# Kernel optimization log

Hardware: AMD Instinct MI355X
Metric: run time of the kernel (lower is better)

## Reference

```python
import jax, jax.numpy as jnp
import numpy as np

N_SAMPLES = 32768   # exp.n_samples = 2**15
N_FRAMES = 128      # exp.n_frames = n_samples // 256
N_EVENTS = 16
MODEL_DIM = 128
N_FREQS = 16        # 2*16 + 1 = 33 pos-encoding features
POS_DIM = 2 * N_FREQS + 1


def pos_encoded(n_frames, n_freqs):
    # linear position in [-pi, pi] plus sin/cos at geometrically spaced freqs
    x = np.linspace(-np.pi, np.pi, n_frames, dtype=np.float32)[:, None]
    feats = [x]
    for i in range(n_freqs):
        feats.append(np.sin((2.0 ** i) * x))
        feats.append(np.cos((2.0 ** i) * x))
    return jnp.asarray(np.concatenate(feats, axis=-1))  # (n_frames, 33)


def hard_softmax_st(x):
    # softmax -> one-hot at argmax (value forced to exactly 1.0), straight-through backward
    sm = jax.nn.softmax(x, axis=-1)
    onehot = jax.nn.one_hot(jnp.argmax(sm, axis=-1), x.shape[-1], dtype=x.dtype)
    return sm + jax.lax.stop_gradient(onehot - sm)


def fft_convolve(env, tf):
    n = env.shape[-1]
    env = jnp.pad(env, ((0, 0), (0, 0), (0, n)))
    tf = jnp.pad(tf, ((0, 0), (0, 0), (0, n)))
    spec = jnp.fft.rfft(env, axis=-1, norm='ortho') * jnp.fft.rfft(tf, axis=-1, norm='ortho')
    return jnp.fft.irfft(spec, axis=-1, norm='ortho')[..., :n]


def setup_inputs() -> dict:
    key = jax.random.key(0)
    k1, k2, k3, k4, k5 = jax.random.split(key, 5)
    B = 32
    time_latent = jax.random.normal(k1, (B * N_EVENTS, MODEL_DIM), jnp.float32)
    stems = jax.random.normal(k2, (B, N_EVENTS, N_SAMPLES), jnp.float32)
    targets = jax.random.normal(k3, (B, N_EVENTS, N_SAMPLES), jnp.float32)
    lim = 1.0 / np.sqrt(MODEL_DIM)
    W = jax.random.uniform(k4, (MODEL_DIM, POS_DIM), jnp.float32, -lim, lim)
    b = jax.random.uniform(k5, (POS_DIM,), jnp.float32, -lim, lim)
    return {"time_latent": time_latent, "stems": stems, "targets": targets, "W": W, "b": b}


def reference(time_latent, stems, targets, W, b):
    # to_pos linear projection: (B*E, 128) -> (B*E, 33)
    p = time_latent @ W + b
    p = p / (jnp.linalg.norm(p, axis=-1, keepdims=True) + 1e-8)
    pos = pos_encoded(N_FRAMES, N_FREQS)
    pos = pos / (jnp.linalg.norm(pos, axis=-1, keepdims=True) + 1e-8)
    sim = p @ pos.T                      # (B*E, n_frames)
    sm = hard_softmax_st(sim)            # one-hot forward, softmax backward
    step = N_SAMPLES // N_FRAMES         # 256
    sparse = jnp.zeros((p.shape[0], N_SAMPLES), p.dtype).at[:, ::step].set(sm)
    sparse = sparse.reshape(-1, N_EVENTS, N_SAMPLES)  # (B, 16, 32768)
    return fft_convolve(sparse, stems)
```

## Files before the change

### kernel.cpp

```cpp
#include <hip/hip_runtime.h>
#include <math.h>

#define N_SAMPLES 32768
#define N_FRAMES  128
#define N_EVENTS  16
#define MODEL_DIM 128
#define N_FREQS   16
#define POS_DIM   33
#define N_ROWS    512


__global__ __launch_bounds__(64) void pos_kernel(float* __restrict__ pos_hat) {
    int f = blockIdx.x;
    int j = threadIdx.x;

    __shared__ float s_feat[POS_DIM];
    __shared__ float s_inv;

    double step = (2.0 * M_PI) / 127.0;
    double xd = -M_PI + (double)f * step;
    if (f == N_FRAMES - 1) xd = M_PI;
    float x = (float)xd;

    if (j < POS_DIM) {
        float v;
        if (j == 0) {
            v = x;
        } else {
            int i = (j - 1) >> 1;
            double arg = ldexp((double)x, i);
            v = (j & 1) ? (float)sin(arg) : (float)cos(arg);
        }
        s_feat[j] = v;
    }
    __syncthreads();

    if (j == 0) {
        double nrm = 0.0;
        for (int k = 0; k < POS_DIM; ++k)
            nrm += (double)s_feat[k] * (double)s_feat[k];
        s_inv = 1.0f / ((float)sqrt(nrm) + 1e-8f);
    }
    __syncthreads();

    if (j < POS_DIM) pos_hat[f * POS_DIM + j] = s_feat[j] * s_inv;
}

__global__ __launch_bounds__(128) void argmax_kernel(
    const float* __restrict__ tl,
    const float* __restrict__ W,
    const float* __restrict__ b,
    const float* __restrict__ pos_hat,
    int* __restrict__ dout)
{
    __shared__ float  s_tl[MODEL_DIM];
    __shared__ float  s_p[POS_DIM];
    __shared__ double sv[N_FRAMES];
    __shared__ int    si[N_FRAMES];

    int row = blockIdx.x;
    int t = threadIdx.x;

    s_tl[t] = tl[(size_t)row * MODEL_DIM + t];
    __syncthreads();

    if (t < POS_DIM) {
        double acc = (double)b[t];
        for (int k = 0; k < MODEL_DIM; ++k)
            acc += (double)s_tl[k] * (double)W[k * POS_DIM + t];
        s_p[t] = (float)acc;
    }
    __syncthreads();

    double s = 0.0;
    for (int j = 0; j < POS_DIM; ++j)
        s += (double)s_p[j] * (double)pos_hat[t * POS_DIM + j];

    sv[t] = s;
    si[t] = t;
    __syncthreads();

    for (int off = 64; off > 0; off >>= 1) {
        if (t < off) {
            double ov = sv[t + off];
            int    oi = si[t + off];
            if (ov > sv[t] || (ov == sv[t] && oi < si[t])) {
                sv[t] = ov;
                si[t] = oi;
            }
        }
        __syncthreads();
    }
    if (t == 0) dout[row] = si[0] * (N_SAMPLES / N_FRAMES);
}

__global__ __launch_bounds__(256) void shift_kernel(
    const float* __restrict__ stems,
    const int*   __restrict__ dvals,
    float*       __restrict__ out)
{
    int row = blockIdx.y;
    int t = (blockIdx.x * 256 + threadIdx.x) * 4;
    int d = dvals[row];

    const float4* src = (const float4*)(stems + (size_t)row * N_SAMPLES);
    float4*       dst = (float4*)(out + (size_t)row * N_SAMPLES);

    float4 v;
    if (t >= d) {
        v = src[(t - d) >> 2];
        const float sc = 1.0f / 256.0f;
        v.x *= sc; v.y *= sc; v.z *= sc; v.w *= sc;
    } else {
        v = make_float4(0.f, 0.f, 0.f, 0.f);
    }
    dst[t >> 2] = v;
}

extern "C" void kernel_launch(void* const* d_in, const int* in_sizes, int n_in,
                              void* d_out, int out_size, void* d_ws, size_t ws_size,
                              hipStream_t stream) {
    const float* tl    = (const float*)d_in[0];
    const float* stems = (const float*)d_in[1];
    const float* W     = (const float*)d_in[3];
    const float* b     = (const float*)d_in[4];
    float* out = (float*)d_out;

    float* pos_hat = (float*)d_ws;
    int*   dvals   = (int*)((char*)d_ws + 32768);

    pos_kernel<<<N_FRAMES, 64, 0, stream>>>(pos_hat);
    argmax_kernel<<<N_ROWS, 128, 0, stream>>>(tl, W, b, pos_hat, dvals);
    shift_kernel<<<dim3(N_SAMPLES / (256 * 4), N_ROWS), 256, 0, stream>>>(stems, dvals, out);
}
```

Baseline: 169.7 us.

## Fuse argmax computation into shift kernel, recomputing per split block

Merges the projection/argmax kernel and the shift-copy kernel into one launch of 1024-thread blocks, with SPLIT blocks per row. Each block recomputes the row's argmax (double-precision matvec and reduction) and then copies its quarter of the shifted, scaled stem. This removes one kernel launch and the global round trip for the shift values. In exchange the argmax work is done four times per row, and the copy cannot start until that serial compute finishes within each block.

```diff
diff --git a/kernel.cpp b/kernel.cpp
--- a/kernel.cpp
+++ b/kernel.cpp
@@ -8,6 +8,7 @@
 #define N_FREQS   16
 #define POS_DIM   33
 #define N_ROWS    512
+#define SPLIT     4
 
 
 __global__ __launch_bounds__(64) void pos_kernel(float* __restrict__ pos_hat) {
@@ -46,22 +47,24 @@
     if (j < POS_DIM) pos_hat[f * POS_DIM + j] = s_feat[j] * s_inv;
 }
 
-__global__ __launch_bounds__(128) void argmax_kernel(
+__global__ __launch_bounds__(1024) void fused_kernel(
     const float* __restrict__ tl,
     const float* __restrict__ W,
     const float* __restrict__ b,
     const float* __restrict__ pos_hat,
-    int* __restrict__ dout)
+    const float* __restrict__ stems,
+    float*       __restrict__ out)
 {
     __shared__ float  s_tl[MODEL_DIM];
     __shared__ float  s_p[POS_DIM];
     __shared__ double sv[N_FRAMES];
     __shared__ int    si[N_FRAMES];
+    __shared__ int    s_d;
 
-    int row = blockIdx.x;
+    int row = blockIdx.y;
     int t = threadIdx.x;
 
-    s_tl[t] = tl[(size_t)row * MODEL_DIM + t];
+    if (t < MODEL_DIM) s_tl[t] = tl[(size_t)row * MODEL_DIM + t];
     __syncthreads();
 
     if (t < POS_DIM) {
@@ -72,12 +75,13 @@
     }
     __syncthreads();
 
-    double s = 0.0;
-    for (int j = 0; j < POS_DIM; ++j)
-        s += (double)s_p[j] * (double)pos_hat[t * POS_DIM + j];
-
-    sv[t] = s;
-    si[t] = t;
+    if (t < N_FRAMES) {
+        double s = 0.0;
+        for (int j = 0; j < POS_DIM; ++j)
+            s += (double)s_p[j] * (double)pos_hat[t * POS_DIM + j];
+        sv[t] = s;
+        si[t] = t;
+    }
     __syncthreads();
 
     for (int off = 64; off > 0; off >>= 1) {
@@ -91,30 +95,27 @@
         }
         __syncthreads();
     }
-    if (t == 0) dout[row] = si[0] * (N_SAMPLES / N_FRAMES);
-}
+    if (t == 0) s_d = si[0] * (N_SAMPLES / N_FRAMES);
+    __syncthreads();
 
-__global__ __launch_bounds__(256) void shift_kernel(
-    const float* __restrict__ stems,
-    const int*   __restrict__ dvals,
-    float*       __restrict__ out)
-{
-    int row = blockIdx.y;
-    int t = (blockIdx.x * 256 + threadIdx.x) * 4;
-    int d = dvals[row];
-
+    int d = s_d;
     const float4* src = (const float4*)(stems + (size_t)row * N_SAMPLES);
     float4*       dst = (float4*)(out + (size_t)row * N_SAMPLES);
+    const float sc = 1.0f / 256.0f;
 
-    float4 v;
-    if (t >= d) {
-        v = src[(t - d) >> 2];
-        const float sc = 1.0f / 256.0f;
-        v.x *= sc; v.y *= sc; v.z *= sc; v.w *= sc;
-    } else {
-        v = make_float4(0.f, 0.f, 0.f, 0.f);
+    int base = blockIdx.x * (N_SAMPLES / SPLIT);
+#pragma unroll
+    for (int it = 0; it < (N_SAMPLES / SPLIT) / (1024 * 4); ++it) {
+        int tt = base + (it * 1024 + t) * 4;
+        float4 v;
+        if (tt >= d) {
+            v = src[(tt - d) >> 2];
+            v.x *= sc; v.y *= sc; v.z *= sc; v.w *= sc;
+        } else {
+            v = make_float4(0.f, 0.f, 0.f, 0.f);
+        }
+        dst[tt >> 2] = v;
     }
-    dst[t >> 2] = v;
 }
 
 extern "C" void kernel_launch(void* const* d_in, const int* in_sizes, int n_in,
@@ -127,9 +128,7 @@
     float* out = (float*)d_out;
 
     float* pos_hat = (float*)d_ws;
-    int*   dvals   = (int*)((char*)d_ws + 32768);
 
     pos_kernel<<<N_FRAMES, 64, 0, stream>>>(pos_hat);
-    argmax_kernel<<<N_ROWS, 128, 0, stream>>>(tl, W, b, pos_hat, dvals);
-    shift_kernel<<<dim3(N_SAMPLES / (256 * 4), N_ROWS), 256, 0, stream>>>(stems, dvals, out);
+    fused_kernel<<<dim3(SPLIT, N_ROWS), 1024, 0, stream>>>(tl, W, b, pos_hat, stems, out);
 }
```

Measured after the change: 182.9 us. 1.08x slower.
